# Optimization experiments

Hardware: AMD Instinct MI355X
Metric: run time of the kernel (lower is better)

The kernel has to match this reference:

```python
import jax, jax.numpy as jnp
import numpy as np
from jax import lax

BN_EPS = 1e-5

def _binarize(t):
    # deterministic sign binarization (sign(0)=0, matching torch.sign)
    return jnp.sign(t)

def setup_inputs() -> dict:
    key = jax.random.key(0)
    k1, k2 = jax.random.split(key)
    N, C, H, W = 16, 128, 128, 128
    x = jax.random.normal(k1, (N, C, H, W), dtype=jnp.float32)
    weight = jax.random.normal(k2, (C, C, 3, 3), dtype=jnp.float32)  # OIHW
    gamma = jnp.ones((C,), dtype=jnp.float32)
    beta = jnp.zeros((C,), dtype=jnp.float32)
    return {"x": x, "weight": weight, "gamma": gamma, "beta": beta}

def reference(x, weight, gamma, beta):
    residual = x
    # binarize activations (C != 3 path) and weights
    bx = _binarize(x)
    bw = _binarize(weight)
    # 3x3 conv, stride 1, padding 1, no bias
    out = lax.conv_general_dilated(
        bx, bw,
        window_strides=(1, 1),
        padding=((1, 1), (1, 1)),
        dimension_numbers=("NCHW", "OIHW", "NCHW"),
    )
    # BatchNorm2d in training mode: batch stats over (N, H, W), biased variance
    mean = jnp.mean(out, axis=(0, 2, 3))
    var = jnp.var(out, axis=(0, 2, 3))
    inv = lax.rsqrt(var + BN_EPS)
    out = (out - mean[None, :, None, None]) * (inv * gamma)[None, :, None, None] + beta[None, :, None, None]
    # Hardtanh
    out = jnp.clip(out, -1.0, 1.0)
    return out + residual
```

## Files before the change

kernel.cpp:

```cpp
#include <hip/hip_runtime.h>
#include <stdint.h>

#define Nn 16
#define Cc 128
#define Hh 128
#define Ww 128
#define HWc (Hh*Ww)
#define NHW 262144

#define ROWP 17408
#define NROW 130
#define XGRP 2176

#define PIXB 132

typedef int v4i  __attribute__((ext_vector_type(4)));
typedef int v16i __attribute__((ext_vector_type(16)));

typedef __attribute__((address_space(3))) unsigned int lds_uint;
typedef __attribute__((address_space(1))) const unsigned int glob_uint;

__device__ __forceinline__ void gload_lds16(const void* g, void* l) {
    __builtin_amdgcn_global_load_lds((glob_uint*)g, (lds_uint*)l, 16, 0, 0);
}

__global__ __launch_bounds__(256) void pack_x(const float* __restrict__ x,
                                              char* __restrict__ x8) {
    int bid = blockIdx.x;
    int n = bid / NROW, r = bid % NROW;
    char* row = x8 + (size_t)bid * ROWP;
    int t = threadIdx.x;

    if (r == 0 || r == NROW - 1) {
        for (int i = t; i < ROWP / 16; i += 256)
            ((uint4*)row)[i] = make_uint4(0, 0, 0, 0);
        return;
    }
    int h = r - 1;
    if (t < 16) {
        int g = t >> 1, p = (t & 1) ? 129 : 0;
        *(uint4*)(row + g * XGRP + p * 16) = make_uint4(0, 0, 0, 0);
    }

    __shared__ char tile[128 * PIXB];
    const float* px = x + (((size_t)n * Cc) * Hh + h) * Ww;
    int w = t & 127, ch = t >> 7;
    for (int q = 0; q < 16; ++q) {
        int c = ch * 64 + q * 4;
        uint32_t d = 0;
        #pragma unroll
        for (int j = 0; j < 4; ++j) {
            float v = px[(size_t)(c + j) * HWc + w];
            int8_t s = (v > 0.f) ? 1 : ((v < 0.f) ? -1 : 0);
            d |= (uint32_t)(uint8_t)s << (8 * j);
        }
        *(uint32_t*)(tile + w * PIXB + c) = d;
    }
    __syncthreads();
    for (int s = 0; s < 4; ++s) {
        int idx = s * 256 + t;
        int w2 = idx & 127, g = idx >> 7;
        const uint32_t* src = (const uint32_t*)(tile + w2 * PIXB + g * 16);
        uint32_t* dst = (uint32_t*)(row + g * XGRP + (1 + w2) * 16);
        dst[0] = src[0]; dst[1] = src[1]; dst[2] = src[2]; dst[3] = src[3];
    }
}

__global__ __launch_bounds__(256) void pack_w(const float* __restrict__ wt,
                                              char* __restrict__ wswz) {
    int gid = blockIdx.x * 256 + threadIdx.x;
    if (gid >= 9216) return;
    int lane = gid & 63, grp = gid >> 6;
    int kh = grp & 3, tap = (grp >> 2) % 9, ot = grp / 36;
    int o  = ot * 32 + (lane & 31);
    int cb = kh * 32 + (lane >> 5) * 16;
    uint32_t dw4[4];
    #pragma unroll
    for (int di = 0; di < 4; ++di) {
        uint32_t d = 0;
        #pragma unroll
        for (int j = 0; j < 4; ++j) {
            int c = cb + di * 4 + j;
            float v = wt[((size_t)o * Cc + c) * 9 + tap];
            int8_t s = (v > 0.f) ? 1 : ((v < 0.f) ? -1 : 0);
            d |= (uint32_t)(uint8_t)s << (8 * j);
        }
        dw4[di] = d;
    }
    *(uint4*)(wswz + (size_t)gid * 16) = make_uint4(dw4[0], dw4[1], dw4[2], dw4[3]);
}

template <typename OutT>
__global__ __launch_bounds__(256) void conv_mfma2(const char* __restrict__ x8,
                                                  const char* __restrict__ wswz,
                                                  OutT* __restrict__ out) {
    __shared__ char lds[3 * ROWP];
    int bid0 = blockIdx.x;
    int bid = (bid0 & 7) * 256 + (bid0 >> 3);
    int n = bid >> 7, h = bid & 127;
    int tid = threadIdx.x, lane = tid & 63, wid = tid >> 6;

    const char* gbase = x8 + ((size_t)n * NROW + h) * ROWP;
    for (int task = wid; task < 51; task += 4) {
        int rr = task / 17, ck = task % 17;
        gload_lds16(gbase + (size_t)rr * ROWP + ck * 1024 + lane * 16,
                    lds + rr * ROWP + ck * 1024);
    }
    __syncthreads();

    int wy = wid >> 1, wx = wid & 1;
    int ln31 = lane & 31, lq = lane >> 5;

    v16i acc[2][2];
    #pragma unroll
    for (int oi = 0; oi < 2; ++oi)
        #pragma unroll
        for (int pi = 0; pi < 2; ++pi)
            #pragma unroll
            for (int r2 = 0; r2 < 16; ++r2) acc[oi][pi][r2] = 0;

    const char* wb0 = wswz + (size_t)(wy * 2 * 9) * 4096 + lane * 16;
    const char* lb  = lds + (size_t)(1 + wx * 64 + ln31) * 16 + lq * XGRP;

    #pragma unroll
    for (int tap = 0; tap < 9; ++tap) {
        int rr = tap / 3, dw = tap % 3 - 1;
        v4i a0[4], a1[4];
        #pragma unroll
        for (int kh = 0; kh < 4; ++kh) {
            a0[kh] = *(const v4i*)(wb0 + (tap * 4 + kh) * 1024);
            a1[kh] = *(const v4i*)(wb0 + (36 + tap * 4 + kh) * 1024);
        }
        const char* pb = lb + rr * ROWP + dw * 16;
        #pragma unroll
        for (int kh = 0; kh < 4; ++kh) {
            v4i b0 = *(const v4i*)(pb + kh * (2 * XGRP));
            v4i b1 = *(const v4i*)(pb + kh * (2 * XGRP) + 512);
            acc[0][0] = __builtin_amdgcn_mfma_i32_32x32x32_i8(a0[kh], b0, acc[0][0], 0, 0, 0);
            acc[0][1] = __builtin_amdgcn_mfma_i32_32x32x32_i8(a0[kh], b1, acc[0][1], 0, 0, 0);
            acc[1][0] = __builtin_amdgcn_mfma_i32_32x32x32_i8(a1[kh], b0, acc[1][0], 0, 0, 0);
            acc[1][1] = __builtin_amdgcn_mfma_i32_32x32x32_i8(a1[kh], b1, acc[1][1], 0, 0, 0);
        }
    }

    OutT* po = out + ((size_t)n * Cc) * HWc + (size_t)h * Ww;
    #pragma unroll
    for (int oi = 0; oi < 2; ++oi)
        #pragma unroll
        for (int pi = 0; pi < 2; ++pi) {
            int wcol = wx * 64 + pi * 32 + ln31;
            #pragma unroll
            for (int r2 = 0; r2 < 16; ++r2) {
                int orow = wy * 64 + oi * 32 + (r2 & 3) + 8 * (r2 >> 2) + 4 * lq;
                po[(size_t)orow * HWc + wcol] = (OutT)acc[oi][pi][r2];
            }
        }
}

__global__ __launch_bounds__(256) void stats16(const short* __restrict__ conv,
                                               unsigned long long* __restrict__ stats) {
    int b = blockIdx.x;
    int c = b & 127, n = b >> 7;
    const uint4* p = (const uint4*)(conv + (size_t)(n * Cc + c) * HWc);
    int sum = 0, sq = 0;
    for (int i = threadIdx.x; i < HWc / 8; i += 256) {
        uint4 v = p[i];
        uint32_t ua[4] = {v.x, v.y, v.z, v.w};
        #pragma unroll
        for (int j = 0; j < 4; ++j) {
            int s0 = (short)(ua[j] & 0xffff), s1 = (short)(ua[j] >> 16);
            sum += s0 + s1;
            sq  += s0 * s0 + s1 * s1;
        }
    }
    #pragma unroll
    for (int off = 32; off > 0; off >>= 1) {
        sum += __shfl_down(sum, off);
        sq  += __shfl_down(sq, off);
    }
    __shared__ int wsum[4], wsq[4];
    int wave = threadIdx.x >> 6, lane = threadIdx.x & 63;
    if (lane == 0) { wsum[wave] = sum; wsq[wave] = sq; }
    __syncthreads();
    if (threadIdx.x == 0) {
        long long S = 0, Q = 0;
        #pragma unroll
        for (int i = 0; i < 4; ++i) { S += wsum[i]; Q += wsq[i]; }
        atomicAdd(&stats[c],       (unsigned long long)S);
        atomicAdd(&stats[128 + c], (unsigned long long)Q);
    }
}

__global__ __launch_bounds__(256) void statsf(const float* __restrict__ conv,
                                              unsigned long long* __restrict__ stats) {
    int b = blockIdx.x;
    int c = b & 127, n = b >> 7;
    const float4* p = (const float4*)(conv + (size_t)(n * Cc + c) * HWc);
    int sum = 0, sq = 0;
    for (int i = threadIdx.x; i < HWc / 4; i += 256) {
        float4 v = p[i];
        int a = (int)v.x, d = (int)v.y, e = (int)v.z, f = (int)v.w;
        sum += a + d + e + f;
        sq  += a * a + d * d + e * e + f * f;
    }
    #pragma unroll
    for (int off = 32; off > 0; off >>= 1) {
        sum += __shfl_down(sum, off);
        sq  += __shfl_down(sq, off);
    }
    __shared__ int wsum[4], wsq[4];
    int wave = threadIdx.x >> 6, lane = threadIdx.x & 63;
    if (lane == 0) { wsum[wave] = sum; wsq[wave] = sq; }
    __syncthreads();
    if (threadIdx.x == 0) {
        long long S = 0, Q = 0;
        #pragma unroll
        for (int i = 0; i < 4; ++i) { S += wsum[i]; Q += wsq[i]; }
        atomicAdd(&stats[c],       (unsigned long long)S);
        atomicAdd(&stats[128 + c], (unsigned long long)Q);
    }
}

__device__ __forceinline__ void bn_coef(const unsigned long long* stats,
                                        const float* gamma, const float* beta,
                                        int c, float& scale, float& shift) {
    long long S = (long long)stats[c];
    long long Q = (long long)stats[128 + c];
    double m   = (double)S / (double)NHW;
    double var = (double)Q / (double)NHW - m * m;
    float inv  = (float)(1.0 / sqrt(var + 1e-5));
    scale = inv * gamma[c];
    shift = beta[c] - (float)m * scale;
}

__global__ __launch_bounds__(256) void apply16(float* __restrict__ out,
                                               const short* __restrict__ conv,
                                               const float* __restrict__ x,
                                               const unsigned long long* __restrict__ stats,
                                               const float* __restrict__ gamma,
                                               const float* __restrict__ beta) {
    int b = blockIdx.x;
    int c = b & 127, n = b >> 7;
    size_t basei = (size_t)(n * Cc + c) * HWc;
    float scale, shift;
    bn_coef(stats, gamma, beta, c, scale, shift);

    const uint4*  pc = (const uint4*)(conv + basei);
    const float4* px = (const float4*)(x + basei);
    float4*       po = (float4*)(out + basei);
    for (int i = threadIdx.x; i < HWc / 8; i += 256) {
        uint4 v = pc[i];
        uint32_t ua[4] = {v.x, v.y, v.z, v.w};
        #pragma unroll
        for (int half = 0; half < 2; ++half) {
            float4 r = px[i * 2 + half];
            float4 o;
            float c0 = (float)(short)(ua[half * 2]     & 0xffff);
            float c1 = (float)(short)(ua[half * 2]     >> 16);
            float c2 = (float)(short)(ua[half * 2 + 1] & 0xffff);
            float c3 = (float)(short)(ua[half * 2 + 1] >> 16);
            o.x = fminf(fmaxf(c0 * scale + shift, -1.0f), 1.0f) + r.x;
            o.y = fminf(fmaxf(c1 * scale + shift, -1.0f), 1.0f) + r.y;
            o.z = fminf(fmaxf(c2 * scale + shift, -1.0f), 1.0f) + r.z;
            o.w = fminf(fmaxf(c3 * scale + shift, -1.0f), 1.0f) + r.w;
            po[i * 2 + half] = o;
        }
    }
}

__global__ __launch_bounds__(256) void applyf(float* __restrict__ out,
                                              const float* __restrict__ x,
                                              const unsigned long long* __restrict__ stats,
                                              const float* __restrict__ gamma,
                                              const float* __restrict__ beta) {
    int b = blockIdx.x;
    int c = b & 127, n = b >> 7;
    size_t basei = (size_t)(n * Cc + c) * HWc;
    float scale, shift;
    bn_coef(stats, gamma, beta, c, scale, shift);

    float4* po = (float4*)(out + basei);
    const float4* px = (const float4*)(x + basei);
    for (int i = threadIdx.x; i < HWc / 4; i += 256) {
        float4 v = po[i];
        float4 r = px[i];
        v.x = fminf(fmaxf(v.x * scale + shift, -1.0f), 1.0f) + r.x;
        v.y = fminf(fmaxf(v.y * scale + shift, -1.0f), 1.0f) + r.y;
        v.z = fminf(fmaxf(v.z * scale + shift, -1.0f), 1.0f) + r.z;
        v.w = fminf(fmaxf(v.w * scale + shift, -1.0f), 1.0f) + r.w;
        po[i] = v;
    }
}

extern "C" void kernel_launch(void* const* d_in, const int* in_sizes, int n_in,
                              void* d_out, int out_size, void* d_ws, size_t ws_size,
                              hipStream_t stream) {
    const float* x     = (const float*)d_in[0];
    const float* wt    = (const float*)d_in[1];
    const float* gamma = (const float*)d_in[2];
    const float* beta  = (const float*)d_in[3];
    float* out = (float*)d_out;

    char* ws = (char*)d_ws;
    unsigned long long* stats = (unsigned long long*)ws;
    char* wswz = ws + 4096;
    char* x8   = ws + 262144;
    const size_t x8_bytes = (size_t)Nn * NROW * ROWP;
    short* conv16 = (short*)(ws + 262144 + x8_bytes);
    const size_t need16 = 262144 + x8_bytes + (size_t)NHW * Cc * 2;

    hipMemsetAsync(stats, 0, 2048, stream);
    pack_x<<<Nn * NROW, 256, 0, stream>>>(x, x8);
    pack_w<<<36, 256, 0, stream>>>(wt, wswz);

    if (ws_size >= need16) {
        conv_mfma2<short><<<Nn * Hh, 256, 0, stream>>>(x8, wswz, conv16);
        stats16<<<Nn * Cc, 256, 0, stream>>>(conv16, stats);
        apply16<<<Nn * Cc, 256, 0, stream>>>(out, conv16, x, stats, gamma, beta);
    } else {
        conv_mfma2<float><<<Nn * Hh, 256, 0, stream>>>(x8, wswz, out);
        statsf<<<Nn * Cc, 256, 0, stream>>>(out, stats);
        applyf<<<Nn * Cc, 256, 0, stream>>>(out, x, stats, gamma, beta);
    }
}
```

Baseline: 352.2 us.

## Fuse BN statistics into conv epilogue via LDS-staged tile and partial sums

The int16 conv epilogue now stages results in LDS, writes them out as coalesced 16-byte rows, and computes per-channel sum and sum-of-squares partials for each (n,h) row. A small reduce_stats kernel replaces the full stats16 pass, so the int16 conv tensor is no longer re-read from global memory for statistics. pack_x is also changed to use float4 loads across four channels at a time. The cost is extra LDS traffic, two barriers in the conv kernel, and a 2 MB partials buffer in the workspace.

New measurement: 350.2 us. About the same (-0.5%).

```diff
diff --git a/kernel.cpp b/kernel.cpp
--- a/kernel.cpp
+++ b/kernel.cpp
@@ -13,6 +13,7 @@
 #define XGRP 2176
 
 #define PIXB 132
+#define TPITCH 136
 
 typedef int v4i  __attribute__((ext_vector_type(4)));
 typedef int v16i __attribute__((ext_vector_type(16)));
@@ -22,6 +23,11 @@
 
 __device__ __forceinline__ void gload_lds16(const void* g, void* l) {
     __builtin_amdgcn_global_load_lds((glob_uint*)g, (lds_uint*)l, 16, 0, 0);
+}
+
+__device__ __forceinline__ uint32_t sgn8(float v) {
+    int8_t s = (v > 0.f) ? 1 : ((v < 0.f) ? -1 : 0);
+    return (uint32_t)(uint8_t)s;
 }
 
 __global__ __launch_bounds__(256) void pack_x(const float* __restrict__ x,
@@ -42,19 +48,26 @@
         *(uint4*)(row + g * XGRP + p * 16) = make_uint4(0, 0, 0, 0);
     }
 
-    __shared__ char tile[128 * PIXB];
+    __shared__ __align__(16) char tile[128 * PIXB];
     const float* px = x + (((size_t)n * Cc) * Hh + h) * Ww;
-    int w = t & 127, ch = t >> 7;
-    for (int q = 0; q < 16; ++q) {
-        int c = ch * 64 + q * 4;
-        uint32_t d = 0;
-        #pragma unroll
-        for (int j = 0; j < 4; ++j) {
-            float v = px[(size_t)(c + j) * HWc + w];
-            int8_t s = (v > 0.f) ? 1 : ((v < 0.f) ? -1 : 0);
-            d |= (uint32_t)(uint8_t)s << (8 * j);
-        }
-        *(uint32_t*)(tile + w * PIXB + c) = d;
+
+    int wq = t & 31, cgb = t >> 5;
+    int w0 = wq * 4;
+    #pragma unroll
+    for (int s = 0; s < 4; ++s) {
+        int c0 = (cgb + 8 * s) * 4;
+        float4 v[4];
+        #pragma unroll
+        for (int j = 0; j < 4; ++j)
+            v[j] = *(const float4*)&px[(size_t)(c0 + j) * HWc + w0];
+        #pragma unroll
+        for (int i = 0; i < 4; ++i) {
+            uint32_t d = sgn8(((const float*)&v[0])[i])
+                       | (sgn8(((const float*)&v[1])[i]) << 8)
+                       | (sgn8(((const float*)&v[2])[i]) << 16)
+                       | (sgn8(((const float*)&v[3])[i]) << 24);
+            *(uint32_t*)(tile + (w0 + i) * PIXB + c0) = d;
+        }
     }
     __syncthreads();
     for (int s = 0; s < 4; ++s) {
@@ -82,8 +95,7 @@
         for (int j = 0; j < 4; ++j) {
             int c = cb + di * 4 + j;
             float v = wt[((size_t)o * Cc + c) * 9 + tap];
-            int8_t s = (v > 0.f) ? 1 : ((v < 0.f) ? -1 : 0);
-            d |= (uint32_t)(uint8_t)s << (8 * j);
+            d |= sgn8(v) << (8 * j);
         }
         dw4[di] = d;
     }
@@ -93,8 +105,9 @@
 template <typename OutT>
 __global__ __launch_bounds__(256) void conv_mfma2(const char* __restrict__ x8,
                                                   const char* __restrict__ wswz,
-                                                  OutT* __restrict__ out) {
-    __shared__ char lds[3 * ROWP];
+                                                  OutT* __restrict__ out,
+                                                  int2* __restrict__ partials) {
+    __shared__ __align__(16) char lds[3 * ROWP];
     int bid0 = blockIdx.x;
     int bid = (bid0 & 7) * 256 + (bid0 >> 3);
     int n = bid >> 7, h = bid & 127;
@@ -144,50 +157,82 @@
     }
 
     OutT* po = out + ((size_t)n * Cc) * HWc + (size_t)h * Ww;
-    #pragma unroll
-    for (int oi = 0; oi < 2; ++oi)
-        #pragma unroll
-        for (int pi = 0; pi < 2; ++pi) {
-            int wcol = wx * 64 + pi * 32 + ln31;
+
+    if constexpr (sizeof(OutT) == 2) {
+        __syncthreads();
+        short* tileS = (short*)lds;
+        #pragma unroll
+        for (int oi = 0; oi < 2; ++oi)
             #pragma unroll
-            for (int r2 = 0; r2 < 16; ++r2) {
-                int orow = wy * 64 + oi * 32 + (r2 & 3) + 8 * (r2 >> 2) + 4 * lq;
-                po[(size_t)orow * HWc + wcol] = (OutT)acc[oi][pi][r2];
+            for (int pi = 0; pi < 2; ++pi) {
+                int wcol = wx * 64 + pi * 32 + ln31;
+                #pragma unroll
+                for (int r2 = 0; r2 < 16; ++r2) {
+                    int orow = wy * 64 + oi * 32 + (r2 & 3) + 8 * (r2 >> 2) + 4 * lq;
+                    tileS[orow * TPITCH + wcol] = (short)acc[oi][pi][r2];
+                }
             }
-        }
-}
-
-__global__ __launch_bounds__(256) void stats16(const short* __restrict__ conv,
-                                               unsigned long long* __restrict__ stats) {
-    int b = blockIdx.x;
-    int c = b & 127, n = b >> 7;
-    const uint4* p = (const uint4*)(conv + (size_t)(n * Cc + c) * HWc);
-    int sum = 0, sq = 0;
-    for (int i = threadIdx.x; i < HWc / 8; i += 256) {
-        uint4 v = p[i];
-        uint32_t ua[4] = {v.x, v.y, v.z, v.w};
-        #pragma unroll
-        for (int j = 0; j < 4; ++j) {
-            int s0 = (short)(ua[j] & 0xffff), s1 = (short)(ua[j] >> 16);
-            sum += s0 + s1;
-            sq  += s0 * s0 + s1 * s1;
-        }
+        __syncthreads();
+        for (int idx = tid; idx < 2048; idx += 256) {
+            int c = idx >> 4, k = idx & 15;
+            *(uint4*)(po + (size_t)c * HWc + k * 8) =
+                *(const uint4*)(tileS + c * TPITCH + k * 8);
+        }
+        int c = tid >> 1, half = tid & 1;
+        const short* rp = tileS + c * TPITCH + half * 64;
+        int S = 0, Q = 0;
+        #pragma unroll
+        for (int k = 0; k < 8; ++k) {
+            int4 vv = *(const int4*)(rp + k * 8);
+            int ua[4] = {vv.x, vv.y, vv.z, vv.w};
+            #pragma unroll
+            for (int j = 0; j < 4; ++j) {
+                int s0 = (short)(ua[j] & 0xffff), s1 = (short)(ua[j] >> 16);
+                S += s0 + s1;
+                Q += s0 * s0 + s1 * s1;
+            }
+        }
+        S += __shfl_xor(S, 1);
+        Q += __shfl_xor(Q, 1);
+        if (half == 0) partials[(size_t)bid * 128 + c] = make_int2(S, Q);
+    } else {
+        #pragma unroll
+        for (int oi = 0; oi < 2; ++oi)
+            #pragma unroll
+            for (int pi = 0; pi < 2; ++pi) {
+                int wcol = wx * 64 + pi * 32 + ln31;
+                #pragma unroll
+                for (int r2 = 0; r2 < 16; ++r2) {
+                    int orow = wy * 64 + oi * 32 + (r2 & 3) + 8 * (r2 >> 2) + 4 * lq;
+                    po[(size_t)orow * HWc + wcol] = (OutT)acc[oi][pi][r2];
+                }
+            }
+    }
+}
+
+__global__ __launch_bounds__(256) void reduce_stats(const int2* __restrict__ partials,
+                                                    unsigned long long* __restrict__ stats) {
+    int c = blockIdx.x;
+    long long S = 0, Q = 0;
+    for (int i = threadIdx.x; i < Nn * Hh; i += 256) {
+        int2 v = partials[(size_t)i * 128 + c];
+        S += v.x; Q += v.y;
     }
     #pragma unroll
     for (int off = 32; off > 0; off >>= 1) {
-        sum += __shfl_down(sum, off);
-        sq  += __shfl_down(sq, off);
-    }
-    __shared__ int wsum[4], wsq[4];
+        S += __shfl_down(S, off);
+        Q += __shfl_down(Q, off);
+    }
+    __shared__ long long sS[4], sQ[4];
     int wave = threadIdx.x >> 6, lane = threadIdx.x & 63;
-    if (lane == 0) { wsum[wave] = sum; wsq[wave] = sq; }
+    if (lane == 0) { sS[wave] = S; sQ[wave] = Q; }
     __syncthreads();
     if (threadIdx.x == 0) {
-        long long S = 0, Q = 0;
-        #pragma unroll
-        for (int i = 0; i < 4; ++i) { S += wsum[i]; Q += wsq[i]; }
-        atomicAdd(&stats[c],       (unsigned long long)S);
-        atomicAdd(&stats[128 + c], (unsigned long long)Q);
+        long long St = 0, Qt = 0;
+        #pragma unroll
+        for (int i = 0; i < 4; ++i) { St += sS[i]; Qt += sQ[i]; }
+        stats[c]       = (unsigned long long)St;
+        stats[128 + c] = (unsigned long long)Qt;
     }
 }
 
@@ -304,21 +349,22 @@
     char* ws = (char*)d_ws;
     unsigned long long* stats = (unsigned long long*)ws;
     char* wswz = ws + 4096;
-    char* x8   = ws + 262144;
+    int2* partials = (int2*)(ws + 262144);
+    char* x8   = ws + 262144 + 2097152;
     const size_t x8_bytes = (size_t)Nn * NROW * ROWP;
-    short* conv16 = (short*)(ws + 262144 + x8_bytes);
-    const size_t need16 = 262144 + x8_bytes + (size_t)NHW * Cc * 2;
+    short* conv16 = (short*)(ws + 262144 + 2097152 + x8_bytes);
+    const size_t need16 = 262144 + 2097152 + x8_bytes + (size_t)NHW * Cc * 2;
 
     hipMemsetAsync(stats, 0, 2048, stream);
     pack_x<<<Nn * NROW, 256, 0, stream>>>(x, x8);
     pack_w<<<36, 256, 0, stream>>>(wt, wswz);
 
     if (ws_size >= need16) {
-        conv_mfma2<short><<<Nn * Hh, 256, 0, stream>>>(x8, wswz, conv16);
-        stats16<<<Nn * Cc, 256, 0, stream>>>(conv16, stats);
+        conv_mfma2<short><<<Nn * Hh, 256, 0, stream>>>(x8, wswz, conv16, partials);
+        reduce_stats<<<Cc, 256, 0, stream>>>(partials, stats);
         apply16<<<Nn * Cc, 256, 0, stream>>>(out, conv16, x, stats, gamma, beta);
     } else {
-        conv_mfma2<float><<<Nn * Hh, 256, 0, stream>>>(x8, wswz, out);
+        conv_mfma2<float><<<Nn * Hh, 256, 0, stream>>>(x8, wswz, out, partials);
         statsf<<<Nn * Cc, 256, 0, stream>>>(out, stats);
         applyf<<<Nn * Cc, 256, 0, stream>>>(out, x, stats, gamma, beta);
     }
```
